# Optimization experiments

Measured on AMD Instinct MI355X. Metric: run time of the kernel, lower is better.

The kernel has to match this reference:

```python
import jax, jax.numpy as jnp
import numpy as np

B, S, H = 64, 2048, 1024
NEG = -1e10


def setup_inputs() -> dict:
    key = jax.random.key(0)
    k1, k2, k3, k4, k5, k6 = jax.random.split(key, 6)
    scale = 1.0 / np.sqrt(2 * H)
    return {
        "decoder_hidden": jax.random.normal(k1, (B, H), dtype=jnp.float32),
        "encoder_outputs": jax.random.normal(k2, (B, S, H), dtype=jnp.float32),
        "mask": jax.random.randint(k3, (B, S), 0, 2, dtype=jnp.int32),
        "W_attn": jax.random.normal(k4, (2 * H, H), dtype=jnp.float32) * scale,
        "b_attn": jax.random.normal(k5, (H,), dtype=jnp.float32) * scale,
        "v_w": jax.random.normal(k6, (H,), dtype=jnp.float32) * (1.0 / np.sqrt(H)),
    }


def reference(decoder_hidden, encoder_outputs, mask, W_attn, b_attn, v_w):
    # concat((dec_rep, enc), -1) @ W_attn == dec @ W_attn[:H] + enc @ W_attn[H:]
    Wd, We = W_attn[:H], W_attn[H:]
    dec_proj = decoder_hidden @ Wd            # [B, H]
    enc_proj = jnp.einsum('bsh,hk->bsk', encoder_outputs, We)  # [B, S, H]
    energy = jnp.tanh(dec_proj[:, None, :] + enc_proj + b_attn)  # [B, S, H]
    attention = jnp.einsum('bsh,h->bs', energy, v_w)             # [B, S]
    attention = jnp.where(mask == 1, NEG, attention)
    return jax.nn.softmax(attention, axis=1)
```

## Files before the change

kernel.cpp:

```cpp
#include <hip/hip_runtime.h>
#include <hip/hip_bf16.h>
#include <stdint.h>

#define HD   1024
#define BB   64
#define SS   2048
#define MT   (BB*SS)
#define NEGV -10000000000.0f

typedef __attribute__((ext_vector_type(8))) short bf16x8;
typedef __attribute__((ext_vector_type(4))) float f32x4;
typedef __attribute__((ext_vector_type(4))) int   i32x4;

__device__ __forceinline__ void gll16(const void* g, void* l) {
  __builtin_amdgcn_global_load_lds((const __attribute__((address_space(1))) void*)g,
                                   (__attribute__((address_space(3))) void*)l, 16, 0, 0);
}

__device__ __forceinline__ float tanh_fast(float x) {
  float e = __expf(2.0f * x);
  return 1.0f - 2.0f / (e + 1.0f);
}


__global__ void prep_we(const float* __restrict__ Wattn, __hip_bfloat16* __restrict__ out) {
  __shared__ float st[64][132];
  int tid = threadIdx.x;
  int nt = blockIdx.x >> 4, kc = blockIdx.x & 15;
  const float* src = Wattn + (size_t)(HD + kc*64)*HD + nt*128;
  #pragma unroll 4
  for (int i = 0; i < 32; ++i) {
    int s = i*256 + tid;
    int kk = s >> 7, nn = s & 127;
    st[kk][nn] = src[(size_t)kk*HD + nn];
  }
  __syncthreads();
  size_t base = (size_t)blockIdx.x * 8192;
  #pragma unroll 4
  for (int i = 0; i < 32; ++i) {
    int lin = i*256 + tid;
    int nl = lin >> 6, j = (lin >> 3) & 7, e = lin & 7;
    int kk = ((j ^ (nl & 7)) << 3) + e;
    out[base + lin] = __float2bfloat16(st[kk][nl]);
  }
}

__global__ void prep_E(const float* __restrict__ E, __hip_bfloat16* __restrict__ out) {
  int tid = threadIdx.x;
  int mt = blockIdx.x >> 4, kc = blockIdx.x & 15;
  const float* src = E + ((size_t)mt*128)*HD + kc*64;
  __hip_bfloat16* dst = out + (size_t)blockIdx.x * 8192;
  #pragma unroll
  for (int i = 0; i < 4; ++i) {
    int u = i*256 + tid;
    int ml = u >> 3, j = u & 7;
    int sk = ((j ^ (ml & 7)) << 3);
    const float* p = src + (size_t)ml*HD + sk;
    f32x4 v0 = *(const f32x4*)p;
    f32x4 v1 = *(const f32x4*)(p + 4);
    union { __hip_bfloat162 h[4]; i32x4 q; } cv;
    cv.h[0] = __float22bfloat162_rn(make_float2(v0.x, v0.y));
    cv.h[1] = __float22bfloat162_rn(make_float2(v0.z, v0.w));
    cv.h[2] = __float22bfloat162_rn(make_float2(v1.x, v1.y));
    cv.h[3] = __float22bfloat162_rn(make_float2(v1.z, v1.w));
    *(i32x4*)(dst + (size_t)u*8) = cv.q;
  }
}

__global__ void prep_dpb(const float* __restrict__ dec, const float* __restrict__ Wattn,
                         const float* __restrict__ battn, float* __restrict__ dpb) {
  __shared__ float red[4][64];
  int b = blockIdx.y, n0 = blockIdx.x*64;
  int nn = threadIdx.x & 63, kg = threadIdx.x >> 6;
  const float* wp = Wattn + (size_t)(kg*256)*HD + n0 + nn;
  const float* dp = dec + b*HD + kg*256;
  float acc = 0.0f;
  #pragma unroll 8
  for (int h = 0; h < 256; ++h) acc += dp[h] * wp[(size_t)h*HD];
  red[kg][nn] = acc;
  __syncthreads();
  if (threadIdx.x < 64) {
    int n = n0 + threadIdx.x;
    dpb[b*HD + n] = battn[n] + red[0][threadIdx.x] + red[1][threadIdx.x]
                             + red[2][threadIdx.x] + red[3][threadIdx.x];
  }
}

__device__ __forceinline__ void decode_bid(int bid, int& bm, int& bn) {
  int x = bid & 7, r = bid >> 3;
  bm = x*128 + (r >> 3);
  bn = r & 7;
}

__global__ void __launch_bounds__(256) gemm_fused_bf(
    const __hip_bfloat16* __restrict__ At, const __hip_bfloat16* __restrict__ Wt,
    const float* __restrict__ dpb, const float* __restrict__ vw,
    float* __restrict__ logits) {
  __shared__ __align__(16) short Al[128*64];
  __shared__ __align__(16) short Bl[128*64];
  __shared__ float red[128];

  int tid = threadIdx.x;
  int lane = tid & 63, wid = tid >> 6;
  int wm = wid & 1, wn = wid >> 1;
  int bm, bn; decode_bid(blockIdx.x, bm, bn);
  int m0 = bm << 7, n0 = bn << 7;
  int lane15 = lane & 15, kg = lane >> 4;

  f32x4 acc[4][4];
  #pragma unroll
  for (int a = 0; a < 4; ++a)
    #pragma unroll
    for (int c = 0; c < 4; ++c) acc[a][c] = (f32x4){0.f, 0.f, 0.f, 0.f};

  for (int kc = 0; kc < 16; ++kc) {
    const char* at = (const char*)At + ((size_t)(bm*16 + kc) * 8192) * 2;
    const char* bt = (const char*)Wt + ((size_t)(bn*16 + kc) * 8192) * 2;
    #pragma unroll
    for (int i = 0; i < 4; ++i) {
      int segbase = (wid*4 + i) * 64;
      gll16(at + (size_t)(segbase + lane)*16, (char*)Al + segbase*16);
      gll16(bt + (size_t)(segbase + lane)*16, (char*)Bl + segbase*16);
    }
    __syncthreads();
    #pragma unroll
    for (int kh = 0; kh < 2; ++kh) {
      bf16x8 af[4], bfr[4];
      #pragma unroll
      for (int mf = 0; mf < 4; ++mf) {
        int row = wm*64 + mf*16 + lane15;
        int jj = kh*4 + kg;
        af[mf] = *(const bf16x8*)&Al[row*64 + ((jj ^ (row & 7)) << 3)];
      }
      #pragma unroll
      for (int nf = 0; nf < 4; ++nf) {
        int nl = wn*64 + nf*16 + lane15;
        int jj = kh*4 + kg;
        bfr[nf] = *(const bf16x8*)&Bl[nl*64 + ((jj ^ (nl & 7)) << 3)];
      }
      #pragma unroll
      for (int mf = 0; mf < 4; ++mf)
        #pragma unroll
        for (int nf = 0; nf < 4; ++nf)
          acc[mf][nf] = __builtin_amdgcn_mfma_f32_16x16x32_bf16(af[mf], bfr[nf], acc[mf][nf], 0, 0, 0);
    }
    __syncthreads();
  }

  int bidx = m0 >> 11;
  float dpv[4], vwv[4];
  #pragma unroll
  for (int nf = 0; nf < 4; ++nf) {
    int n = n0 + wn*64 + nf*16 + lane15;
    dpv[nf] = dpb[bidx*HD + n];
    vwv[nf] = vw[n];
  }
  if (tid < 128) red[tid] = 0.0f;
  __syncthreads();
  #pragma unroll
  for (int mf = 0; mf < 4; ++mf) {
    #pragma unroll
    for (int r = 0; r < 4; ++r) {
      float s = 0.0f;
      #pragma unroll
      for (int nf = 0; nf < 4; ++nf) {
        float x = acc[mf][nf][r] + dpv[nf];
        s += tanh_fast(x) * vwv[nf];
      }
      s += __shfl_xor(s, 1); s += __shfl_xor(s, 2);
      s += __shfl_xor(s, 4); s += __shfl_xor(s, 8);
      if (lane15 == 0) atomicAdd(&red[wm*64 + mf*16 + kg*4 + r], s);
    }
  }
  __syncthreads();
  if (tid < 128) atomicAdd(&logits[m0 + tid], red[tid]);
}

__global__ void __launch_bounds__(256) gemm_fused_f32(
    const float* __restrict__ E, const __hip_bfloat16* __restrict__ Wt,
    const float* __restrict__ dpb, const float* __restrict__ vw,
    float* __restrict__ logits) {
  __shared__ __align__(16) short Al[128*72];
  __shared__ __align__(16) short Bl[128*64];
  __shared__ float red[128];

  int tid = threadIdx.x;
  int lane = tid & 63, wid = tid >> 6;
  int wm = wid & 1, wn = wid >> 1;
  int bm, bn; decode_bid(blockIdx.x, bm, bn);
  int m0 = bm << 7, n0 = bn << 7;
  int lane15 = lane & 15, kg = lane >> 4;

  f32x4 acc[4][4];
  #pragma unroll
  for (int a = 0; a < 4; ++a)
    #pragma unroll
    for (int c = 0; c < 4; ++c) acc[a][c] = (f32x4){0.f, 0.f, 0.f, 0.f};

  for (int kc = 0; kc < 16; ++kc) {
    const char* bt = (const char*)Wt + ((size_t)(bn*16 + kc) * 8192) * 2;
    #pragma unroll
    for (int i = 0; i < 4; ++i) {
      int segbase = (wid*4 + i) * 64;
      gll16(bt + (size_t)(segbase + lane)*16, (char*)Bl + segbase*16);
    }
    const float* Eg = E + (m0*HD + kc*64);
    #pragma unroll
    for (int i = 0; i < 8; ++i) {
      int s = i*256 + tid;
      int r = s >> 4, q = s & 15;
      f32x4 v = *(const f32x4*)(Eg + r*HD + q*4);
      union { __hip_bfloat162 h[2]; unsigned long long u; } cv;
      cv.h[0] = __float22bfloat162_rn(make_float2(v.x, v.y));
      cv.h[1] = __float22bfloat162_rn(make_float2(v.z, v.w));
      *(unsigned long long*)&Al[r*72 + q*4] = cv.u;
    }
    __syncthreads();
    #pragma unroll
    for (int kh = 0; kh < 2; ++kh) {
      bf16x8 af[4], bfr[4];
      #pragma unroll
      for (int mf = 0; mf < 4; ++mf) {
        int row = wm*64 + mf*16 + lane15;
        af[mf] = *(const bf16x8*)&Al[row*72 + kh*32 + kg*8];
      }
      #pragma unroll
      for (int nf = 0; nf < 4; ++nf) {
        int nl = wn*64 + nf*16 + lane15;
        int jj = kh*4 + kg;
        bfr[nf] = *(const bf16x8*)&Bl[nl*64 + ((jj ^ (nl & 7)) << 3)];
      }
      #pragma unroll
      for (int mf = 0; mf < 4; ++mf)
        #pragma unroll
        for (int nf = 0; nf < 4; ++nf)
          acc[mf][nf] = __builtin_amdgcn_mfma_f32_16x16x32_bf16(af[mf], bfr[nf], acc[mf][nf], 0, 0, 0);
    }
    __syncthreads();
  }

  int bidx = m0 >> 11;
  float dpv[4], vwv[4];
  #pragma unroll
  for (int nf = 0; nf < 4; ++nf) {
    int n = n0 + wn*64 + nf*16 + lane15;
    dpv[nf] = dpb[bidx*HD + n];
    vwv[nf] = vw[n];
  }
  if (tid < 128) red[tid] = 0.0f;
  __syncthreads();
  #pragma unroll
  for (int mf = 0; mf < 4; ++mf) {
    #pragma unroll
    for (int r = 0; r < 4; ++r) {
      float s = 0.0f;
      #pragma unroll
      for (int nf = 0; nf < 4; ++nf) {
        float x = acc[mf][nf][r] + dpv[nf];
        s += tanh_fast(x) * vwv[nf];
      }
      s += __shfl_xor(s, 1); s += __shfl_xor(s, 2);
      s += __shfl_xor(s, 4); s += __shfl_xor(s, 8);
      if (lane15 == 0) atomicAdd(&red[wm*64 + mf*16 + kg*4 + r], s);
    }
  }
  __syncthreads();
  if (tid < 128) atomicAdd(&logits[m0 + tid], red[tid]);
}

__global__ void softmax_k(const float* __restrict__ logits, const int* __restrict__ mask,
                          float* __restrict__ out) {
  __shared__ float smax[4];
  __shared__ float ssum[4];
  int tid = threadIdx.x, lane = tid & 63, wid = tid >> 6;
  int b = blockIdx.x;
  const float* lg = logits + b*SS;
  const int*   mk = mask   + b*SS;
  f32x4 l0 = *(const f32x4*)(lg + tid*8);
  f32x4 l1 = *(const f32x4*)(lg + tid*8 + 4);
  i32x4 q0 = *(const i32x4*)(mk + tid*8);
  i32x4 q1 = *(const i32x4*)(mk + tid*8 + 4);
  float v[8];
  v[0] = (q0.x == 1) ? NEGV : l0.x;  v[1] = (q0.y == 1) ? NEGV : l0.y;
  v[2] = (q0.z == 1) ? NEGV : l0.z;  v[3] = (q0.w == 1) ? NEGV : l0.w;
  v[4] = (q1.x == 1) ? NEGV : l1.x;  v[5] = (q1.y == 1) ? NEGV : l1.y;
  v[6] = (q1.z == 1) ? NEGV : l1.z;  v[7] = (q1.w == 1) ? NEGV : l1.w;
  float mx = v[0];
  #pragma unroll
  for (int i = 1; i < 8; ++i) mx = fmaxf(mx, v[i]);
  #pragma unroll
  for (int m = 1; m <= 32; m <<= 1) mx = fmaxf(mx, __shfl_xor(mx, m));
  if (lane == 0) smax[wid] = mx;
  __syncthreads();
  mx = fmaxf(fmaxf(smax[0], smax[1]), fmaxf(smax[2], smax[3]));
  float s = 0.0f;
  #pragma unroll
  for (int i = 0; i < 8; ++i) { v[i] = __expf(v[i] - mx); s += v[i]; }
  #pragma unroll
  for (int m = 1; m <= 32; m <<= 1) s += __shfl_xor(s, m);
  if (lane == 0) ssum[wid] = s;
  __syncthreads();
  s = ssum[0] + ssum[1] + ssum[2] + ssum[3];
  float inv = 1.0f / s;
  f32x4 o0 = {v[0]*inv, v[1]*inv, v[2]*inv, v[3]*inv};
  f32x4 o1 = {v[4]*inv, v[5]*inv, v[6]*inv, v[7]*inv};
  *(f32x4*)(out + b*SS + tid*8)     = o0;
  *(f32x4*)(out + b*SS + tid*8 + 4) = o1;
}

extern "C" void kernel_launch(void* const* d_in, const int* in_sizes, int n_in,
                              void* d_out, int out_size, void* d_ws, size_t ws_size,
                              hipStream_t stream) {
  const float* dec   = (const float*)d_in[0];
  const float* enc   = (const float*)d_in[1];
  const int*   mask  = (const int*)  d_in[2];
  const float* Wattn = (const float*)d_in[3];
  const float* battn = (const float*)d_in[4];
  const float* vw    = (const float*)d_in[5];
  float* out = (float*)d_out;

  const size_t EBF_BYTES = (size_t)MT * HD * 2;
  const size_t FAST_NEED = EBF_BYTES + (2u<<20) + (256u<<10) + (512u<<10);

  char* ws = (char*)d_ws;
  if (ws_size >= FAST_NEED) {
    __hip_bfloat16* ebf = (__hip_bfloat16*)ws;
    __hip_bfloat16* wet = (__hip_bfloat16*)(ws + EBF_BYTES);
    float* dpb    = (float*)(ws + EBF_BYTES + (2u<<20));
    float* logits = (float*)(ws + EBF_BYTES + (2u<<20) + (256u<<10));

    prep_E <<<16384, 256, 0, stream>>>(enc, ebf);
    prep_we<<<128, 256, 0, stream>>>(Wattn, wet);
    prep_dpb<<<dim3(16, 64), 256, 0, stream>>>(dec, Wattn, battn, dpb);
    hipMemsetAsync(logits, 0, (size_t)MT*sizeof(float), stream);
    gemm_fused_bf<<<8192, 256, 0, stream>>>(ebf, wet, dpb, vw, logits);
    softmax_k<<<BB, 256, 0, stream>>>(logits, mask, out);
  } else {
    __hip_bfloat16* wet = (__hip_bfloat16*)ws;
    float* dpb    = (float*)(ws + (2u<<20));
    float* logits = (float*)(ws + (2u<<20) + (256u<<10));

    prep_we<<<128, 256, 0, stream>>>(Wattn, wet);
    prep_dpb<<<dim3(16, 64), 256, 0, stream>>>(dec, Wattn, battn, dpb);
    hipMemsetAsync(logits, 0, (size_t)MT*sizeof(float), stream);
    gemm_fused_f32<<<8192, 256, 0, stream>>>(enc, wet, dpb, vw, logits);
    softmax_k<<<BB, 256, 0, stream>>>(logits, mask, out);
  }
}
```

Measured before the change: 1.202 ms.

## Loop over all N tiles per block to drop global atomics and memset

The fused bf16 GEMM now gives each block one 128-row M tile and loops over all eight N tiles inside the block. It keeps per-row partial sums of the tanh·v products in registers and writes logits directly, with no global atomicAdd and no memset. The grid shrinks from 8192 to 1024 blocks. On a 256-CU part that means only about four waves of long blocks, and the E tile is reloaded from global/L2 for each N tile with no reuse across them.

New measurement: 1.450 ms. +20.6%, slower.

```diff
diff --git a/kernel.cpp b/kernel.cpp
--- a/kernel.cpp
+++ b/kernel.cpp
@@ -86,13 +86,7 @@
   }
 }
 
-__device__ __forceinline__ void decode_bid(int bid, int& bm, int& bn) {
-  int x = bid & 7, r = bid >> 3;
-  bm = x*128 + (r >> 3);
-  bn = r & 7;
-}
-
-__global__ void __launch_bounds__(256) gemm_fused_bf(
+__global__ void __launch_bounds__(256) gemm_mono(
     const __hip_bfloat16* __restrict__ At, const __hip_bfloat16* __restrict__ Wt,
     const float* __restrict__ dpb, const float* __restrict__ vw,
     float* __restrict__ logits) {
@@ -103,77 +97,96 @@
   int tid = threadIdx.x;
   int lane = tid & 63, wid = tid >> 6;
   int wm = wid & 1, wn = wid >> 1;
-  int bm, bn; decode_bid(blockIdx.x, bm, bn);
-  int m0 = bm << 7, n0 = bn << 7;
+  int bm = blockIdx.x;
+  int m0 = bm << 7;
   int lane15 = lane & 15, kg = lane >> 4;
-
-  f32x4 acc[4][4];
+  int bidx = m0 >> 11;
+
+  float rowsum[4][4];
   #pragma unroll
   for (int a = 0; a < 4; ++a)
     #pragma unroll
-    for (int c = 0; c < 4; ++c) acc[a][c] = (f32x4){0.f, 0.f, 0.f, 0.f};
-
-  for (int kc = 0; kc < 16; ++kc) {
-    const char* at = (const char*)At + ((size_t)(bm*16 + kc) * 8192) * 2;
-    const char* bt = (const char*)Wt + ((size_t)(bn*16 + kc) * 8192) * 2;
-    #pragma unroll
-    for (int i = 0; i < 4; ++i) {
-      int segbase = (wid*4 + i) * 64;
-      gll16(at + (size_t)(segbase + lane)*16, (char*)Al + segbase*16);
-      gll16(bt + (size_t)(segbase + lane)*16, (char*)Bl + segbase*16);
-    }
-    __syncthreads();
-    #pragma unroll
-    for (int kh = 0; kh < 2; ++kh) {
-      bf16x8 af[4], bfr[4];
-      #pragma unroll
-      for (int mf = 0; mf < 4; ++mf) {
-        int row = wm*64 + mf*16 + lane15;
+    for (int c = 0; c < 4; ++c) rowsum[a][c] = 0.0f;
+  if (tid < 128) red[tid] = 0.0f;
+
+  for (int bn = 0; bn < 8; ++bn) {
+    f32x4 acc[4][4];
+    #pragma unroll
+    for (int a = 0; a < 4; ++a)
+      #pragma unroll
+      for (int c = 0; c < 4; ++c) acc[a][c] = (f32x4){0.f, 0.f, 0.f, 0.f};
+
+    for (int kc = 0; kc < 16; ++kc) {
+      const char* at = (const char*)At + ((size_t)(bm*16 + kc) * 8192) * 2;
+      const char* bt = (const char*)Wt + ((size_t)(bn*16 + kc) * 8192) * 2;
+      #pragma unroll
+      for (int i = 0; i < 4; ++i) {
+        int segbase = (wid*4 + i) * 64;
+        gll16(at + (size_t)(segbase + lane)*16, (char*)Al + segbase*16);
+        gll16(bt + (size_t)(segbase + lane)*16, (char*)Bl + segbase*16);
+      }
+      __syncthreads();
+      #pragma unroll
+      for (int kh = 0; kh < 2; ++kh) {
+        bf16x8 af[4], bfr[4];
         int jj = kh*4 + kg;
-        af[mf] = *(const bf16x8*)&Al[row*64 + ((jj ^ (row & 7)) << 3)];
-      }
-      #pragma unroll
-      for (int nf = 0; nf < 4; ++nf) {
-        int nl = wn*64 + nf*16 + lane15;
-        int jj = kh*4 + kg;
-        bfr[nf] = *(const bf16x8*)&Bl[nl*64 + ((jj ^ (nl & 7)) << 3)];
-      }
-      #pragma unroll
-      for (int mf = 0; mf < 4; ++mf)
-        #pragma unroll
-        for (int nf = 0; nf < 4; ++nf)
-          acc[mf][nf] = __builtin_amdgcn_mfma_f32_16x16x32_bf16(af[mf], bfr[nf], acc[mf][nf], 0, 0, 0);
-    }
-    __syncthreads();
-  }
-
-  int bidx = m0 >> 11;
-  float dpv[4], vwv[4];
-  #pragma unroll
-  for (int nf = 0; nf < 4; ++nf) {
-    int n = n0 + wn*64 + nf*16 + lane15;
-    dpv[nf] = dpb[bidx*HD + n];
-    vwv[nf] = vw[n];
-  }
-  if (tid < 128) red[tid] = 0.0f;
-  __syncthreads();
-  #pragma unroll
-  for (int mf = 0; mf < 4; ++mf) {
+        #pragma unroll
+        for (int mf = 0; mf < 4; ++mf) {
+          int row = wm*64 + mf*16 + lane15;
+          af[mf] = *(const bf16x8*)&Al[row*64 + ((jj ^ (row & 7)) << 3)];
+        }
+        #pragma unroll
+        for (int nf = 0; nf < 4; ++nf) {
+          int nl = wn*64 + nf*16 + lane15;
+          bfr[nf] = *(const bf16x8*)&Bl[nl*64 + ((jj ^ (nl & 7)) << 3)];
+        }
+        #pragma unroll
+        for (int mf = 0; mf < 4; ++mf)
+          #pragma unroll
+          for (int nf = 0; nf < 4; ++nf)
+            acc[mf][nf] = __builtin_amdgcn_mfma_f32_16x16x32_bf16(af[mf], bfr[nf], acc[mf][nf], 0, 0, 0);
+      }
+      __syncthreads();
+    }
+
+    float dpv[4], vwv[4];
+    #pragma unroll
+    for (int nf = 0; nf < 4; ++nf) {
+      int n = bn*128 + wn*64 + nf*16 + lane15;
+      dpv[nf] = dpb[bidx*HD + n];
+      vwv[nf] = vw[n];
+    }
+    #pragma unroll
+    for (int mf = 0; mf < 4; ++mf)
+      #pragma unroll
+      for (int r = 0; r < 4; ++r) {
+        float s = 0.0f;
+        #pragma unroll
+        for (int nf = 0; nf < 4; ++nf) {
+          float x = acc[mf][nf][r] + dpv[nf];
+          s += tanh_fast(x) * vwv[nf];
+        }
+        rowsum[mf][r] += s;
+      }
+  }
+
+  #pragma unroll
+  for (int mf = 0; mf < 4; ++mf)
     #pragma unroll
     for (int r = 0; r < 4; ++r) {
-      float s = 0.0f;
-      #pragma unroll
-      for (int nf = 0; nf < 4; ++nf) {
-        float x = acc[mf][nf][r] + dpv[nf];
-        s += tanh_fast(x) * vwv[nf];
-      }
+      float s = rowsum[mf][r];
       s += __shfl_xor(s, 1); s += __shfl_xor(s, 2);
       s += __shfl_xor(s, 4); s += __shfl_xor(s, 8);
       if (lane15 == 0) atomicAdd(&red[wm*64 + mf*16 + kg*4 + r], s);
     }
-  }
-  __syncthreads();
-  if (tid < 128) atomicAdd(&logits[m0 + tid], red[tid]);
+  __syncthreads();
+  if (tid < 128) logits[m0 + tid] = red[tid];
+}
+
+__device__ __forceinline__ void decode_bid(int bid, int& bm, int& bn) {
+  int x = bid & 7, r = bid >> 3;
+  bm = x*128 + (r >> 3);
+  bn = r & 7;
 }
 
 __global__ void __launch_bounds__(256) gemm_fused_f32(
@@ -332,8 +345,7 @@
     prep_E <<<16384, 256, 0, stream>>>(enc, ebf);
     prep_we<<<128, 256, 0, stream>>>(Wattn, wet);
     prep_dpb<<<dim3(16, 64), 256, 0, stream>>>(dec, Wattn, battn, dpb);
-    hipMemsetAsync(logits, 0, (size_t)MT*sizeof(float), stream);
-    gemm_fused_bf<<<8192, 256, 0, stream>>>(ebf, wet, dpb, vw, logits);
+    gemm_mono<<<1024, 256, 0, stream>>>(ebf, wet, dpb, vw, logits);
     softmax_k<<<BB, 256, 0, stream>>>(logits, mask, out);
   } else {
     __hip_bfloat16* wet = (__hip_bfloat16*)ws;
```
